# Optimization experiments

Measured on AMD Instinct MI355X. Metric: run time of the kernel, lower is better.

Reference implementation:

```python
import jax, jax.numpy as jnp
import numpy as np

N_NODES = 100000
N_EDGES = 1600000
NUM_FEATURES = 48
HIDDEN = 256
NUM_CLASSES = 1


def setup_inputs() -> dict:
    key = jax.random.key(0)
    k1, k2, k3, k4 = jax.random.split(key, 4)
    x = jax.random.normal(k1, (N_NODES, NUM_FEATURES), dtype=jnp.float32)
    edge_index = jax.random.randint(k2, (2, N_EDGES), 0, N_NODES, dtype=jnp.int32)
    W1 = jax.random.normal(k3, (NUM_FEATURES, HIDDEN), dtype=jnp.float32) / np.sqrt(NUM_FEATURES)
    W2 = jax.random.normal(k4, (HIDDEN, NUM_CLASSES), dtype=jnp.float32) / np.sqrt(HIDDEN)
    bias = jnp.zeros((NUM_CLASSES,), dtype=jnp.float32)
    b2 = jnp.zeros((NUM_CLASSES,), dtype=jnp.float32)
    return {"x": x, "edge_index": edge_index, "W1": W1, "bias": bias, "W2": W2, "b2": b2}


def _gcn_propagate(x, edge_index, num_nodes):
    # Add self-loops.
    loop = jnp.arange(num_nodes, dtype=edge_index.dtype)
    row = jnp.concatenate([edge_index[0], loop])  # source nodes
    col = jnp.concatenate([edge_index[1], loop])  # destination nodes
    # Symmetric normalization D^{-1/2} A D^{-1/2}.
    ones = jnp.ones(col.shape[0], dtype=x.dtype)
    deg = jax.ops.segment_sum(ones, col, num_segments=num_nodes)
    dinv = jax.lax.rsqrt(jnp.maximum(deg, 1.0))
    norm = dinv[row] * dinv[col]  # [E+N]
    # Gather-scale-scatter: memory-bound edge aggregation.
    msg = x[row] * norm[:, None]  # [E+N, F]
    return jax.ops.segment_sum(msg, col, num_segments=num_nodes)  # [N, F]


def reference(x, edge_index, W1, bias, W2, b2):
    h = _gcn_propagate(x, edge_index, x.shape[0])  # [N, F]
    h = h @ W1 + bias                               # [N, H] (+ broadcast bias, C==1)
    h = h @ W2 + b2                                 # [N, C]
    return h
```

## Files before the change

kernel.cpp:

```cpp
#include <hip/hip_runtime.h>


constexpr int kNodes  = 100000;
constexpr int kEdges  = 1600000;
constexpr int kFeat   = 48;
constexpr int kHidden = 256;

constexpr int kBShift = 9;
constexpr int kBSize  = 1 << kBShift;
constexpr int kNB     = 196;
constexpr int kEPB    = 8192;
constexpr int kQuads  = kEdges / 4;
constexpr int kBBlk   = (kEdges + kEPB - 1) / kEPB;
constexpr int kZBlk   = (kNodes + 511) / 512;
constexpr int kCap    = 10240;
constexpr int kLCap   = 64;
constexpr int kLStr   = 65;
constexpr int kPoison = (int)0xAAAAAAAAu;

__global__ __launch_bounds__(512) void fat_kernel(const int* __restrict__ row,
                                                  const int* __restrict__ col,
                                                  const float* __restrict__ x,
                                                  const float* __restrict__ W1,
                                                  const float* __restrict__ W2,
                                                  int* __restrict__ cursor,
                                                  int* __restrict__ bpacked,
                                                  float* __restrict__ z) {
    __shared__ int   lbuck[kNB * kLStr];
    __shared__ int   lcur[256];
    __shared__ int   gbase[256];
    __shared__ float sw2[kHidden];
    __shared__ float spart[kFeat * 4];
    __shared__ float swv[kFeat];
    const int tid = threadIdx.x;

    if (blockIdx.x < kBBlk) {
        if (tid < 256) lcur[tid] = 0;
        __syncthreads();

        int qbase = blockIdx.x * (kEPB / 4);
        const int4* colq = reinterpret_cast<const int4*>(col);
        const int4* rowq = reinterpret_cast<const int4*>(row);
        #pragma unroll
        for (int k = 0; k < 4; ++k) {
            int q = qbase + k * 512 + tid;
            if (q < kQuads) {
                int4 c = colq[q];
                int4 r = rowq[q];
                int cs[4] = {c.x, c.y, c.z, c.w};
                int rs[4] = {r.x, r.y, r.z, r.w};
                #pragma unroll
                for (int u = 0; u < 4; ++u) {
                    int b  = cs[u] >> kBShift;
                    int pk = ((cs[u] & (kBSize - 1)) << 17) | rs[u];
                    int s  = atomicAdd(&lcur[b], 1);
                    if (s < kLCap) {
                        lbuck[b * kLStr + s] = pk;
                    } else {
                        int g = atomicAdd(&cursor[b], 1) - kPoison;
                        if (g < kCap) bpacked[b * kCap + g] = pk;
                    }
                }
            }
        }
        __syncthreads();
        if (tid < kNB) {
            int cnt = min(lcur[tid], kLCap);
            gbase[tid] = atomicAdd(&cursor[tid], cnt) - kPoison;
        }
        __syncthreads();
        int wave = tid >> 6, lane = tid & 63;
        for (int b = wave; b < kNB; b += 8) {
            int cnt = min(lcur[b], kLCap);
            int g   = gbase[b] + lane;
            if (lane < cnt && g < kCap)
                bpacked[b * kCap + g] = lbuck[b * kLStr + lane];
        }
    } else {
        if (tid < kHidden) sw2[tid] = W2[tid];
        __syncthreads();
        if (tid < kFeat * 4) {
            int t = tid >> 2, q = tid & 3;
            const float4* wr = reinterpret_cast<const float4*>(W1 + t * kHidden + q * 64);
            const float4* b4 = reinterpret_cast<const float4*>(sw2) + q * 16;
            float a = 0.f;
            #pragma unroll
            for (int j = 0; j < 16; ++j) {
                float4 u = wr[j];
                float4 v = b4[j];
                a += u.x * v.x + u.y * v.y + u.z * v.z + u.w * v.w;
            }
            spart[tid] = a;
        }
        __syncthreads();
        if (tid < kFeat)
            swv[tid] = spart[4 * tid] + spart[4 * tid + 1]
                     + spart[4 * tid + 2] + spart[4 * tid + 3];
        __syncthreads();
        int i = (blockIdx.x - kBBlk) * 512 + tid;
        if (i < kNodes) {
            const float4* xp = reinterpret_cast<const float4*>(x + (size_t)i * kFeat);
            float acc = 0.f;
            #pragma unroll
            for (int k = 0; k < kFeat / 4; ++k) {
                float4 v = xp[k];
                acc += v.x * swv[4 * k + 0] + v.y * swv[4 * k + 1]
                     + v.z * swv[4 * k + 2] + v.w * swv[4 * k + 3];
            }
            z[i] = acc;
        }
    }
}

__global__ __launch_bounds__(1024) void degfin_kernel(const int* __restrict__ cursor,
                                                      const int* __restrict__ bpacked,
                                                      const float* __restrict__ z,
                                                      float* __restrict__ dinv,
                                                      float* __restrict__ dy) {
    __shared__ int sdeg[kBSize];
    int b = blockIdx.x, tid = threadIdx.x;
    if (tid < kBSize) sdeg[tid] = 0;
    __syncthreads();
    int n = min(cursor[b] - kPoison, kCap);
    int base = b * kCap;
    const int4* bq = reinterpret_cast<const int4*>(bpacked + base);
    int nq = n >> 2;
    for (int i = tid; i < nq; i += 1024) {
        int4 p = bq[i];
        atomicAdd(&sdeg[p.x >> 17], 1);
        atomicAdd(&sdeg[p.y >> 17], 1);
        atomicAdd(&sdeg[p.z >> 17], 1);
        atomicAdd(&sdeg[p.w >> 17], 1);
    }
    if (tid < (n & 3)) atomicAdd(&sdeg[bpacked[base + (n & ~3) + tid] >> 17], 1);
    __syncthreads();
    int node = b * kBSize + tid;
    if (tid < kBSize && node < kNodes) {
        float d  = (float)(sdeg[tid] + 1);
        float di = rsqrtf(d);
        dinv[node] = di;
        dy[node]   = di * z[node];
    }
}

__global__ __launch_bounds__(1024) void agg_kernel(const int* __restrict__ cursor,
                                                   const int* __restrict__ bpacked,
                                                   const float* __restrict__ dy,
                                                   const float* __restrict__ dinv,
                                                   const float* __restrict__ bias,
                                                   const float* __restrict__ W2,
                                                   const float* __restrict__ b2,
                                                   float* __restrict__ out) {
    __shared__ float ssum[kBSize];
    __shared__ float sc;
    int b = blockIdx.x, tid = threadIdx.x;
    if (tid < kBSize) ssum[tid] = 0.f;
    if (tid < 64) {
        const float4* w2q = reinterpret_cast<const float4*>(W2);
        float4 v = w2q[tid];
        float s = v.x + v.y + v.z + v.w;
        #pragma unroll
        for (int o = 32; o > 0; o >>= 1) s += __shfl_down(s, o);
        if (tid == 0) sc = bias[0] * s + b2[0];
    }
    __syncthreads();
    int n = min(cursor[b] - kPoison, kCap);
    int base = b * kCap;
    const int4* bq = reinterpret_cast<const int4*>(bpacked + base);
    int nq = n >> 2;
    for (int i = tid; i < nq; i += 1024) {
        int4 p = bq[i];
        atomicAdd(&ssum[p.x >> 17], dy[p.x & 0x1FFFF]);
        atomicAdd(&ssum[p.y >> 17], dy[p.y & 0x1FFFF]);
        atomicAdd(&ssum[p.z >> 17], dy[p.z & 0x1FFFF]);
        atomicAdd(&ssum[p.w >> 17], dy[p.w & 0x1FFFF]);
    }
    if (tid < (n & 3)) {
        int p = bpacked[base + (n & ~3) + tid];
        atomicAdd(&ssum[p >> 17], dy[p & 0x1FFFF]);
    }
    __syncthreads();
    int node = b * kBSize + tid;
    if (tid < kBSize && node < kNodes)
        out[node] = dinv[node] * (ssum[tid] + dy[node]) + sc;
}

extern "C" void kernel_launch(void* const* d_in, const int* in_sizes, int n_in,
                              void* d_out, int out_size, void* d_ws, size_t ws_size,
                              hipStream_t stream) {
    const float* x    = (const float*)d_in[0];
    const int*   ei   = (const int*)d_in[1];
    const float* W1   = (const float*)d_in[2];
    const float* bias = (const float*)d_in[3];
    const float* W2   = (const float*)d_in[4];
    const float* b2   = (const float*)d_in[5];
    float*       out  = (float*)d_out;

    const int* row = ei;
    const int* col = ei + kEdges;

    char*  p       = (char*)d_ws;
    int*   cursor  = (int*)p;                   p += 1024;
    float* z       = (float*)p;                 p += (size_t)kNodes * 4;
    float* dinv    = (float*)p;                 p += (size_t)kNodes * 4;
    float* dy      = (float*)p;                 p += (size_t)kNodes * 4;
    int*   bpacked = (int*)p;

    fat_kernel<<<kBBlk + kZBlk, 512, 0, stream>>>(row, col, x, W1, W2, cursor, bpacked, z);
    degfin_kernel<<<kNB, 1024, 0, stream>>>(cursor, bpacked, z, dinv, dy);
    agg_kernel<<<kNB, 1024, 0, stream>>>(cursor, bpacked, dy, dinv, bias, W2, b2, out);
}
```

Measured before the change: 103.7 us.

## Move x·(W1·W2) projection from bucketing kernel into degree-finalize kernel

The per-node projection z = x·(W1 W2) moves out of the edge-bucketing kernel's extra blocks and into the degree-finalize kernel. Each degree block now computes the folded weight vector with its upper threads while the lower threads count degrees, then projects its own 512 nodes directly. This drops the z workspace round trip and the extra blocks in the first kernel. In exchange, the x read (19 MB) now happens in a kernel with only 196 blocks, which may expose memory latency, and the W1·W2 fold is repeated in every block.

After: 108.3 us. 1.04x slower.

```diff
diff --git a/kernel.cpp b/kernel.cpp
--- a/kernel.cpp
+++ b/kernel.cpp
@@ -12,7 +12,6 @@
 constexpr int kEPB    = 8192;
 constexpr int kQuads  = kEdges / 4;
 constexpr int kBBlk   = (kEdges + kEPB - 1) / kEPB;
-constexpr int kZBlk   = (kNodes + 511) / 512;
 constexpr int kCap    = 10240;
 constexpr int kLCap   = 64;
 constexpr int kLStr   = 65;
@@ -20,107 +19,85 @@
 
 __global__ __launch_bounds__(512) void fat_kernel(const int* __restrict__ row,
                                                   const int* __restrict__ col,
-                                                  const float* __restrict__ x,
-                                                  const float* __restrict__ W1,
-                                                  const float* __restrict__ W2,
                                                   int* __restrict__ cursor,
-                                                  int* __restrict__ bpacked,
-                                                  float* __restrict__ z) {
-    __shared__ int   lbuck[kNB * kLStr];
-    __shared__ int   lcur[256];
-    __shared__ int   gbase[256];
+                                                  int* __restrict__ bpacked) {
+    __shared__ int lbuck[kNB * kLStr];
+    __shared__ int lcur[256];
+    __shared__ int gbase[256];
+    const int tid = threadIdx.x;
+
+    if (tid < 256) lcur[tid] = 0;
+    __syncthreads();
+
+    int qbase = blockIdx.x * (kEPB / 4);
+    const int4* colq = reinterpret_cast<const int4*>(col);
+    const int4* rowq = reinterpret_cast<const int4*>(row);
+    #pragma unroll
+    for (int k = 0; k < 4; ++k) {
+        int q = qbase + k * 512 + tid;
+        if (q < kQuads) {
+            int4 c = colq[q];
+            int4 r = rowq[q];
+            int cs[4] = {c.x, c.y, c.z, c.w};
+            int rs[4] = {r.x, r.y, r.z, r.w};
+            #pragma unroll
+            for (int u = 0; u < 4; ++u) {
+                int b  = cs[u] >> kBShift;
+                int pk = ((cs[u] & (kBSize - 1)) << 17) | rs[u];
+                int s  = atomicAdd(&lcur[b], 1);
+                if (s < kLCap) {
+                    lbuck[b * kLStr + s] = pk;
+                } else {
+                    int g = atomicAdd(&cursor[b], 1) - kPoison;
+                    if (g < kCap) bpacked[b * kCap + g] = pk;
+                }
+            }
+        }
+    }
+    __syncthreads();
+    if (tid < kNB) {
+        int cnt = min(lcur[tid], kLCap);
+        gbase[tid] = atomicAdd(&cursor[tid], cnt) - kPoison;
+    }
+    __syncthreads();
+    int wave = tid >> 6, lane = tid & 63;
+    for (int b = wave; b < kNB; b += 8) {
+        int cnt = min(lcur[b], kLCap);
+        int g   = gbase[b] + lane;
+        if (lane < cnt && g < kCap)
+            bpacked[b * kCap + g] = lbuck[b * kLStr + lane];
+    }
+}
+
+__global__ __launch_bounds__(1024) void degfin_kernel(const int* __restrict__ cursor,
+                                                      const int* __restrict__ bpacked,
+                                                      const float* __restrict__ x,
+                                                      const float* __restrict__ W1,
+                                                      const float* __restrict__ W2,
+                                                      float* __restrict__ dinv,
+                                                      float* __restrict__ dy) {
+    __shared__ int   sdeg[kBSize];
     __shared__ float sw2[kHidden];
     __shared__ float spart[kFeat * 4];
     __shared__ float swv[kFeat];
-    const int tid = threadIdx.x;
-
-    if (blockIdx.x < kBBlk) {
-        if (tid < 256) lcur[tid] = 0;
-        __syncthreads();
-
-        int qbase = blockIdx.x * (kEPB / 4);
-        const int4* colq = reinterpret_cast<const int4*>(col);
-        const int4* rowq = reinterpret_cast<const int4*>(row);
+    const int b = blockIdx.x, tid = threadIdx.x;
+    if (tid < kBSize) sdeg[tid] = 0;
+    if (tid >= 512 && tid < 512 + kHidden) sw2[tid - 512] = W2[tid - 512];
+    __syncthreads();
+
+    if (tid >= 512 && tid < 512 + kFeat * 4) {
+        int t = (tid - 512) >> 2, q = tid & 3;
+        const float4* wr = reinterpret_cast<const float4*>(W1 + t * kHidden + q * 64);
+        const float4* b4 = reinterpret_cast<const float4*>(sw2) + q * 16;
+        float a = 0.f;
         #pragma unroll
-        for (int k = 0; k < 4; ++k) {
-            int q = qbase + k * 512 + tid;
-            if (q < kQuads) {
-                int4 c = colq[q];
-                int4 r = rowq[q];
-                int cs[4] = {c.x, c.y, c.z, c.w};
-                int rs[4] = {r.x, r.y, r.z, r.w};
-                #pragma unroll
-                for (int u = 0; u < 4; ++u) {
-                    int b  = cs[u] >> kBShift;
-                    int pk = ((cs[u] & (kBSize - 1)) << 17) | rs[u];
-                    int s  = atomicAdd(&lcur[b], 1);
-                    if (s < kLCap) {
-                        lbuck[b * kLStr + s] = pk;
-                    } else {
-                        int g = atomicAdd(&cursor[b], 1) - kPoison;
-                        if (g < kCap) bpacked[b * kCap + g] = pk;
-                    }
-                }
-            }
+        for (int j = 0; j < 16; ++j) {
+            float4 u = wr[j];
+            float4 v = b4[j];
+            a += u.x * v.x + u.y * v.y + u.z * v.z + u.w * v.w;
         }
-        __syncthreads();
-        if (tid < kNB) {
-            int cnt = min(lcur[tid], kLCap);
-            gbase[tid] = atomicAdd(&cursor[tid], cnt) - kPoison;
-        }
-        __syncthreads();
-        int wave = tid >> 6, lane = tid & 63;
-        for (int b = wave; b < kNB; b += 8) {
-            int cnt = min(lcur[b], kLCap);
-            int g   = gbase[b] + lane;
-            if (lane < cnt && g < kCap)
-                bpacked[b * kCap + g] = lbuck[b * kLStr + lane];
-        }
-    } else {
-        if (tid < kHidden) sw2[tid] = W2[tid];
-        __syncthreads();
-        if (tid < kFeat * 4) {
-            int t = tid >> 2, q = tid & 3;
-            const float4* wr = reinterpret_cast<const float4*>(W1 + t * kHidden + q * 64);
-            const float4* b4 = reinterpret_cast<const float4*>(sw2) + q * 16;
-            float a = 0.f;
-            #pragma unroll
-            for (int j = 0; j < 16; ++j) {
-                float4 u = wr[j];
-                float4 v = b4[j];
-                a += u.x * v.x + u.y * v.y + u.z * v.z + u.w * v.w;
-            }
-            spart[tid] = a;
-        }
-        __syncthreads();
-        if (tid < kFeat)
-            swv[tid] = spart[4 * tid] + spart[4 * tid + 1]
-                     + spart[4 * tid + 2] + spart[4 * tid + 3];
-        __syncthreads();
-        int i = (blockIdx.x - kBBlk) * 512 + tid;
-        if (i < kNodes) {
-            const float4* xp = reinterpret_cast<const float4*>(x + (size_t)i * kFeat);
-            float acc = 0.f;
-            #pragma unroll
-            for (int k = 0; k < kFeat / 4; ++k) {
-                float4 v = xp[k];
-                acc += v.x * swv[4 * k + 0] + v.y * swv[4 * k + 1]
-                     + v.z * swv[4 * k + 2] + v.w * swv[4 * k + 3];
-            }
-            z[i] = acc;
-        }
-    }
-}
-
-__global__ __launch_bounds__(1024) void degfin_kernel(const int* __restrict__ cursor,
-                                                      const int* __restrict__ bpacked,
-                                                      const float* __restrict__ z,
-                                                      float* __restrict__ dinv,
-                                                      float* __restrict__ dy) {
-    __shared__ int sdeg[kBSize];
-    int b = blockIdx.x, tid = threadIdx.x;
-    if (tid < kBSize) sdeg[tid] = 0;
-    __syncthreads();
+        spart[tid - 512] = a;
+    }
     int n = min(cursor[b] - kPoison, kCap);
     int base = b * kCap;
     const int4* bq = reinterpret_cast<const int4*>(bpacked + base);
@@ -134,12 +111,24 @@
     }
     if (tid < (n & 3)) atomicAdd(&sdeg[bpacked[base + (n & ~3) + tid] >> 17], 1);
     __syncthreads();
+    if (tid < kFeat)
+        swv[tid] = spart[4 * tid] + spart[4 * tid + 1]
+                 + spart[4 * tid + 2] + spart[4 * tid + 3];
+    __syncthreads();
     int node = b * kBSize + tid;
     if (tid < kBSize && node < kNodes) {
+        const float4* xp = reinterpret_cast<const float4*>(x + (size_t)node * kFeat);
+        float acc = 0.f;
+        #pragma unroll
+        for (int k = 0; k < kFeat / 4; ++k) {
+            float4 v = xp[k];
+            acc += v.x * swv[4 * k + 0] + v.y * swv[4 * k + 1]
+                 + v.z * swv[4 * k + 2] + v.w * swv[4 * k + 3];
+        }
         float d  = (float)(sdeg[tid] + 1);
         float di = rsqrtf(d);
         dinv[node] = di;
-        dy[node]   = di * z[node];
+        dy[node]   = di * acc;
     }
 }
 
@@ -201,12 +190,11 @@
 
     char*  p       = (char*)d_ws;
     int*   cursor  = (int*)p;                   p += 1024;
-    float* z       = (float*)p;                 p += (size_t)kNodes * 4;
     float* dinv    = (float*)p;                 p += (size_t)kNodes * 4;
     float* dy      = (float*)p;                 p += (size_t)kNodes * 4;
     int*   bpacked = (int*)p;
 
-    fat_kernel<<<kBBlk + kZBlk, 512, 0, stream>>>(row, col, x, W1, W2, cursor, bpacked, z);
-    degfin_kernel<<<kNB, 1024, 0, stream>>>(cursor, bpacked, z, dinv, dy);
+    fat_kernel<<<kBBlk, 512, 0, stream>>>(row, col, cursor, bpacked);
+    degfin_kernel<<<kNB, 1024, 0, stream>>>(cursor, bpacked, x, W1, W2, dinv, dy);
     agg_kernel<<<kNB, 1024, 0, stream>>>(cursor, bpacked, dy, dinv, bias, W2, b2, out);
 }
```
